# Optimization experiments

Hardware: AMD Instinct MI355X
Metric: run time of the kernel (lower is better)

Reference implementation:

```python
import jax, jax.numpy as jnp
import numpy as np
import math

B, S, L, D, H, HID = 8, 512, 6, 512, 8, 2048
N_CITIES, C = 10000, 256
IN_DIM = C + 1  # pretrained out_channels + normalized demand


def setup_inputs() -> dict:
    key = jax.random.key(0)
    ks = jax.random.split(key, 32)
    # solutions: [B,S,4]; col0 = city index (int-valued float), col2 = demand, col3 = capacity state
    idx = jax.random.randint(ks[0], (B, S), 0, N_CITIES).astype(jnp.float32)
    demand = jax.random.uniform(ks[1], (B, S), minval=0.0, maxval=10.0)
    cap_state = jax.random.uniform(ks[2], (B, S), minval=20.0, maxval=100.0)
    solutions = jnp.stack([idx, jnp.zeros((B, S)), demand, cap_state], axis=-1).astype(jnp.float32)
    capacities = jax.random.uniform(ks[3], (B,), minval=50.0, maxval=100.0)

    def lin(k, fi, fo):
        kw, kb = jax.random.split(k)
        return (jax.random.normal(kw, (fi, fo)) / np.float32(math.sqrt(fi)),
                jax.random.normal(kb, (fo,)) * 0.01)

    embeddings = jax.random.normal(ks[4], (N_CITIES, C)) * 0.1
    src_W, src_b = lin(ks[5], IN_DIM, D)
    cand_W, cand_b = lin(ks[6], IN_DIM, D)
    dep_W, dep_b = lin(ks[7], IN_DIM, D)
    feas_W, feas_b = lin(ks[8], D, 1)

    def stack(kk, fi, fo):
        Ws, bs = zip(*[lin(jax.random.fold_in(kk, i), fi, fo) for i in range(L)])
        return jnp.stack(Ws), jnp.stack(bs)

    Wq, bq = stack(ks[9], D, D)
    Wk, bk = stack(ks[10], D, D)
    Wv, bv = stack(ks[11], D, D)
    Wo, bo = stack(ks[12], D, D)
    s_scale = jnp.full((L,), 0.43, dtype=jnp.float32)
    W1, b1 = stack(ks[13], D, HID)
    W2, b2 = stack(ks[14], HID, D)
    ptr_W, ptr_b = lin(ks[15], D, 2)
    return dict(solutions=solutions, capacities=capacities, embeddings=embeddings,
                src_W=src_W, src_b=src_b, cand_W=cand_W, cand_b=cand_b,
                dep_W=dep_W, dep_b=dep_b, feas_W=feas_W, feas_b=feas_b,
                Wq=Wq, bq=bq, Wk=Wk, bk=bk, Wv=Wv, bv=bv, Wo=Wo, bo=bo,
                s_scale=s_scale, W1=W1, b1=b1, W2=W2, b2=b2,
                ptr_W=ptr_W, ptr_b=ptr_b)


def _mha(x, Wq, bq, Wk, bk, Wv, bv, Wo, bo, s):
    b, n, d = x.shape
    hd = d // H
    q = (x @ Wq + bq).reshape(b, n, H, hd)
    k = (x @ Wk + bk).reshape(b, n, H, hd)
    v = (x @ Wv + bv).reshape(b, n, H, hd)
    scores = jnp.einsum('bqhd,bkhd->bhqk', q, k) / np.float32(math.sqrt(hd))
    # ScalableSoftmax: softmax(scores + s * log(n)) over last dim
    w = jax.nn.softmax(scores + s * np.float32(math.log(n)), axis=-1)
    out = jnp.einsum('bhqk,bkhd->bqhd', w, v).reshape(b, n, d)
    return out @ Wo + bo


def _forward(solutions, capacities, embeddings, src_W, src_b, cand_W, cand_b,
             dep_W, dep_b, feas_W, feas_b, Wq, bq, Wk, bk, Wv, bv, Wo, bo,
             s_scale, W1, b1, W2, b2, ptr_W, ptr_b):
    idx = jax.lax.stop_gradient(solutions)[:, :, 0].astype(jnp.int32)  # city indices
    enc = embeddings[idx]                                              # [B,S,C]
    rem = solutions[:, 0, 3]
    nd = 2.0 * ((solutions[:, :, 2] - rem[:, None]) / capacities[:, None])
    xin = jnp.concatenate([enc, nd[..., None]], axis=-1)               # [B,S,C+1]
    xin = xin.at[:, 0, -1].set(0.0)

    # NodeEmbedder: source / candidates / depot with separate linears
    src = xin[:, :1] @ src_W + src_b
    cand = xin[:, 1:-1] @ cand_W + cand_b
    dep = xin[:, -1:] @ dep_W + dep_b
    x = jnp.concatenate([src, cand, dep], axis=1)                      # [B,S,D]

    x = x + _mha(x, Wq[0], bq[0], Wk[0], bk[0], Wv[0], bv[0], Wo[0], bo[0], s_scale[0])
    feas = (x[:, 1:-1] @ feas_W + feas_b)[..., 0]                      # [B,S-2]

    for i in range(L):
        if i > 0:
            x = x + _mha(x, Wq[i], bq[i], Wk[i], bk[i], Wv[i], bv[i], Wo[i], bo[i], s_scale[i])
        x = x + (jax.nn.relu(x @ W1[i] + b1[i]) @ W2[i] + b2[i])

    logits = x @ ptr_W + ptr_b                                         # [B,S,2]
    out = jnp.concatenate([logits[:, 1:-1, 0], logits[:, 1:-1, 1]], axis=1)  # [B,2*(S-2)]
    return out, feas


def reference(solutions, capacities, embeddings, src_W, src_b, cand_W, cand_b,
              dep_W, dep_b, feas_W, feas_b, Wq, bq, Wk, bk, Wv, bv, Wo, bo,
              s_scale, W1, b1, W2, b2, ptr_W, ptr_b):
    return _forward(solutions, capacities, embeddings, src_W, src_b, cand_W, cand_b,
                    dep_W, dep_b, feas_W, feas_b, Wq, bq, Wk, bk, Wv, bv, Wo, bo,
                    s_scale, W1, b1, W2, b2, ptr_W, ptr_b)
```

## Files before the change

### kernel.cpp

```cpp
#include <hip/hip_runtime.h>

typedef unsigned short u16;
typedef _Float16 half8 __attribute__((ext_vector_type(8)));
typedef float f32x4 __attribute__((ext_vector_type(4)));

__device__ inline float bf2f(u16 b) { return __builtin_bit_cast(float, ((unsigned)b) << 16); }
__device__ inline float h2f(u16 h) { return (float)__builtin_bit_cast(_Float16, h); }
__device__ inline u16 f2h_bits(float f) { return __builtin_bit_cast(u16, (_Float16)f); }

__device__ inline int detect_bf16(const void* caps) {
    const u16* c = (const u16*)caps;
    int cnt = 0;
#pragma unroll
    for (int k = 0; k < 4; ++k) {
        float v = bf2f(c[2 * k]);
        if (v >= 20.f && v <= 200.f) cnt++;
    }
    return cnt >= 2;
}
__device__ inline float ldin(const void* p, size_t i, int flag) {
    return flag ? bf2f(((const u16*)p)[i]) : ((const float*)p)[i];
}

#define GLOAD_LDS16(g, l)                                                              \
    __builtin_amdgcn_global_load_lds((__attribute__((address_space(1))) const void*)(g), \
                                     (__attribute__((address_space(3))) void*)(l), 16, 0, 0)

#define A_SRCW 0
#define A_SRCB 131584
#define A_CANDW 132096
#define A_CANDB 263680
#define A_DEPW 264192
#define A_DEPB 395776
#define A_FEASW 396288
#define A_FEASB 396800
#define A_PW 396801
#define A_PB 397825
#define A_BO 397827
#define A_B1 400899
#define A_B2 413187
#define A_TOTAL 416259

template <int CF, int BN>
__global__ __launch_bounds__(256) void gemm_f16(
    const u16* __restrict__ A, int lda,
    const u16* __restrict__ B, int ldb,
    void* __restrict__ Cv, int ldc,
    const float* __restrict__ bias, float* __restrict__ resid,
    u16* __restrict__ vtp,
    float scale, int relu, int N, int K)
{
    constexpr int NT = BN / 32;
    __shared__ __attribute__((aligned(16))) u16 As[2][128 * 32];
    __shared__ __attribute__((aligned(16))) u16 Bs[2][BN * 32];

    const int gx = gridDim.x, gy = gridDim.y;
    int mb, nb;
    if ((gy & 7) == 0) {
        int id = blockIdx.x + blockIdx.y * gx;
        int xcd = id & 7, local = id >> 3;
        int mloc = local / gx;
        mb = xcd * (gy >> 3) + mloc;
        nb = local - mloc * gx;
    } else {
        mb = blockIdx.y;
        nb = blockIdx.x;
    }
    const int m0 = mb * 128;
    const int n0 = nb * BN;

    const int t = threadIdx.x, lane = t & 63, wid = t >> 6;
    const int qd = lane >> 4, ml = lane & 15;
    const int wm = (wid >> 1) * 64, wn = (wid & 1) * (BN / 2);

    f32x4 acc[4][NT] = {};

    auto stage = [&](int bf, int k0) {
#pragma unroll
        for (int rep = 0; rep < 2; ++rep) {
            int seg = (wid + rep * 4) * 64 + lane;
            int row = seg >> 2, c8 = (seg & 3) * 8;
            const u16* ga = A + (long long)(m0 + row) * lda + k0 + c8;
            GLOAD_LDS16(ga, As[bf] + (size_t)(seg & ~63) * 8);
            if (BN == 128 || rep == 0) {
                int rn = n0 + row;
                if (rn > N - 1) rn = N - 1;
                const u16* gb = B + (long long)rn * ldb + k0 + c8;
                GLOAD_LDS16(gb, Bs[bf] + (size_t)(seg & ~63) * 8);
            }
        }
    };

    stage(0, 0);
    __syncthreads();

    int buf = 0;
    for (int k0 = 0; k0 < K; k0 += 32) {
        if (k0 + 32 < K) stage(buf ^ 1, k0 + 32);

        half8 af[4], bfv[NT];
#pragma unroll
        for (int mt = 0; mt < 4; ++mt)
            af[mt] = *(const half8*)(As[buf] + (wm + mt * 16 + ml) * 32 + qd * 8);
#pragma unroll
        for (int nt = 0; nt < NT; ++nt)
            bfv[nt] = *(const half8*)(Bs[buf] + (wn + nt * 16 + ml) * 32 + qd * 8);
#pragma unroll
        for (int mt = 0; mt < 4; ++mt)
#pragma unroll
            for (int nt = 0; nt < NT; ++nt)
                acc[mt][nt] = __builtin_amdgcn_mfma_f32_16x16x32_f16(af[mt], bfv[nt], acc[mt][nt], 0, 0, 0);

        __syncthreads();
        buf ^= 1;
    }

#pragma unroll
    for (int nt = 0; nt < NT; ++nt) {
        int col = n0 + wn + nt * 16 + ml;
        if (col >= N) continue;
        float bv = bias ? bias[col] : 0.f;
#pragma unroll
        for (int mt = 0; mt < 4; ++mt) {
#pragma unroll
            for (int r = 0; r < 4; ++r) {
                int rowg = m0 + wm + mt * 16 + qd * 4 + r;
                float v = acc[mt][nt][r] * scale + bv;
                if (relu) v = fmaxf(v, 0.f);
                long long off = (long long)rowg * ldc + col;
                if (CF == 1) {
                    ((float*)Cv)[off] = v;
                } else if (CF == 2) {
                    resid[off] = v;
                    ((u16*)Cv)[off] = f2h_bits(v);
                } else if (resid) {
                    float nv = resid[off] + v;
                    resid[off] = nv;
                    ((u16*)Cv)[off] = f2h_bits(nv);
                } else if (vtp && col >= 1024) {
                    int b = rowg >> 9, s = rowg & 511;
                    int cv2 = col - 1024;
                    vtp[(size_t)(((b << 3) + (cv2 >> 6)) * 32768 + (cv2 & 63) * 512 + s)] = f2h_bits(v);
                } else {
                    ((u16*)Cv)[off] = f2h_bits(v);
                }
            }
        }
    }
}

__global__ __launch_bounds__(256) void flash_k(
    const u16* __restrict__ qkv,
    const u16* __restrict__ vt,
    u16* __restrict__ ob)
{
    __shared__ __attribute__((aligned(16))) u16 Ps[128 * 136];

    int id = blockIdx.x + (blockIdx.y << 2);
    int xcd = id & 7, local = id >> 3;
    const int z = (xcd << 3) + (local >> 2);
    const int q0 = (local & 3) * 128;

    const int b = z >> 3, h = z & 7;
    const long long qbase = (long long)b * 786432;
    const u16* Q  = qkv + qbase + (long long)q0 * 1536 + h * 64;
    const u16* Kg = qkv + qbase + 512 + h * 64;
    const u16* Vg = vt + (long long)z * 32768;

    const int t = threadIdx.x, lane = t & 63, wid = t >> 6;
    const int qd = lane >> 4, ml = lane & 15;
    const int wm = wid * 32;

    half8 qf[2][2];
#pragma unroll
    for (int mt = 0; mt < 2; ++mt)
#pragma unroll
        for (int kf = 0; kf < 2; ++kf)
            qf[mt][kf] = *(const half8*)(Q + (long long)(wm + mt * 16 + ml) * 1536 + kf * 32 + qd * 8);

    f32x4 oacc[2][4] = {};
    float mrow[2][4], lrow[2][4];
#pragma unroll
    for (int mt = 0; mt < 2; ++mt)
#pragma unroll
        for (int r = 0; r < 4; ++r) { mrow[mt][r] = -3.0e38f; lrow[mt][r] = 0.f; }

    for (int kb = 0; kb < 4; ++kb) {
        f32x4 sacc[2][8] = {};
#pragma unroll
        for (int nt = 0; nt < 8; ++nt) {
#pragma unroll
            for (int kf = 0; kf < 2; ++kf) {
                half8 bf = *(const half8*)(Kg + (long long)(kb * 128 + nt * 16 + ml) * 1536 + kf * 32 + qd * 8);
#pragma unroll
                for (int mt = 0; mt < 2; ++mt)
                    sacc[mt][nt] = __builtin_amdgcn_mfma_f32_16x16x32_f16(qf[mt][kf], bf, sacc[mt][nt], 0, 0, 0);
            }
        }
#pragma unroll
        for (int mt = 0; mt < 2; ++mt) {
#pragma unroll
            for (int r = 0; r < 4; ++r) {
                float mx = -3.0e38f;
#pragma unroll
                for (int nt = 0; nt < 8; ++nt) {
                    float s = sacc[mt][nt][r] * 0.125f;
                    sacc[mt][nt][r] = s;
                    mx = fmaxf(mx, s);
                }
#pragma unroll
                for (int o = 1; o < 16; o <<= 1) mx = fmaxf(mx, __shfl_xor(mx, o, 64));
                float mnew = fmaxf(mrow[mt][r], mx);
                float alpha = __expf(mrow[mt][r] - mnew);
                mrow[mt][r] = mnew;
                lrow[mt][r] *= alpha;
#pragma unroll
                for (int nt = 0; nt < 4; ++nt) oacc[mt][nt][r] *= alpha;
                float ps = 0.f;
#pragma unroll
                for (int nt = 0; nt < 8; ++nt) {
                    float p = __expf(sacc[mt][nt][r] - mnew);
                    sacc[mt][nt][r] = p;
                    ps += p;
                }
#pragma unroll
                for (int o = 1; o < 16; o <<= 1) ps += __shfl_xor(ps, o, 64);
                lrow[mt][r] += ps;
            }
        }
#pragma unroll
        for (int mt = 0; mt < 2; ++mt)
#pragma unroll
            for (int nt = 0; nt < 8; ++nt)
#pragma unroll
                for (int r = 0; r < 4; ++r)
                    Ps[(wm + mt * 16 + qd * 4 + r) * 136 + nt * 16 + ml] = f2h_bits(sacc[mt][nt][r]);
#pragma unroll
        for (int kf = 0; kf < 4; ++kf) {
            half8 pf[2];
#pragma unroll
            for (int mt = 0; mt < 2; ++mt)
                pf[mt] = *(const half8*)(Ps + (wm + mt * 16 + ml) * 136 + kf * 32 + qd * 8);
#pragma unroll
            for (int nt = 0; nt < 4; ++nt) {
                half8 vf = *(const half8*)(Vg + (long long)(nt * 16 + ml) * 512 + kb * 128 + kf * 32 + qd * 8);
#pragma unroll
                for (int mt = 0; mt < 2; ++mt)
                    oacc[mt][nt] = __builtin_amdgcn_mfma_f32_16x16x32_f16(pf[mt], vf, oacc[mt][nt], 0, 0, 0);
            }
        }
    }

#pragma unroll
    for (int mt = 0; mt < 2; ++mt) {
#pragma unroll
        for (int r = 0; r < 4; ++r) {
            float inv = 1.f / lrow[mt][r];
            long long rowg = (long long)b * 512 + q0 + wm + mt * 16 + qd * 4 + r;
#pragma unroll
            for (int nt = 0; nt < 4; ++nt)
                ob[rowg * 512 + h * 64 + nt * 16 + ml] = f2h_bits(oacc[mt][nt][r] * inv);
        }
    }
}

template <int MODE>
__global__ void transpose_k(const void* __restrict__ src_, int s_ld, long long s_off,
                            long long s_so, long long s_si,
                            u16* __restrict__ dst, int d_ld, long long d_so, long long d_si,
                            int R, int Rs, int C, const void* caps)
{
    __shared__ u16 tile[32][33];
    const int z = blockIdx.z;
    const long long sb = s_off + (long long)(z >> 3) * s_so + (long long)(z & 7) * s_si;
    dst += (long long)(z >> 3) * d_so + (long long)(z & 7) * d_si;
    const int c0 = blockIdx.x * 32, r0 = blockIdx.y * 32;
    const int tx = threadIdx.x, ty = threadIdx.y;
    const int flag = (MODE == 1) ? detect_bf16(caps) : 0;
#pragma unroll
    for (int i = 0; i < 4; ++i) {
        int r = r0 + ty + i * 8, c = c0 + tx;
        if (r < R && c < C) {
            u16 v = 0;
            if (r < Rs) {
                size_t idx = (size_t)(sb + (long long)r * s_ld + c);
                if (MODE == 1) v = f2h_bits(ldin(src_, idx, flag));
                else           v = ((const u16*)src_)[idx];
            }
            tile[ty + i * 8][tx] = v;
        }
    }
    __syncthreads();
#pragma unroll
    for (int i = 0; i < 4; ++i) {
        int r = r0 + tx, c = c0 + ty + i * 8;
        if (r < R && c < C) dst[(long long)c * d_ld + r] = tile[tx][ty + i * 8];
    }
}

__global__ void qkvoT6_k(const void* Wq, const void* Wk, const void* Wv, const void* Wo,
                         u16* __restrict__ wqkvT6, u16* __restrict__ woT6,
                         const void* caps)
{
    __shared__ u16 tile[32][33];
    const int z = blockIdx.z;
    const int layer = z >> 2, sel = z & 3;
    const void* src = (sel == 0) ? Wq : (sel == 1) ? Wk : (sel == 2) ? Wv : Wo;
    u16* dst = (sel < 3) ? (wqkvT6 + (long long)layer * 786432 + (long long)sel * 262144)
                         : (woT6 + (long long)layer * 262144);
    const long long oW = (long long)layer * 262144;
    const int c0 = blockIdx.x * 32, r0 = blockIdx.y * 32;
    const int tx = threadIdx.x, ty = threadIdx.y;
    const int flag = detect_bf16(caps);
#pragma unroll
    for (int i = 0; i < 4; ++i) {
        int r = r0 + ty + i * 8, c = c0 + tx;
        tile[ty + i * 8][tx] = f2h_bits(ldin(src, (size_t)(oW + (long long)r * 512 + c), flag));
    }
    __syncthreads();
#pragma unroll
    for (int i = 0; i < 4; ++i) {
        int r = r0 + tx, c = c0 + ty + i * 8;
        dst[(long long)c * 512 + r] = tile[tx][ty + i * 8];
    }
}

__global__ void cvt_small_k(const void* srcW, const void* srcB, const void* candW, const void* candB,
                            const void* depW, const void* depB, const void* feasW, const void* feasB,
                            const void* pW, const void* pb, const void* boi, const void* b1i,
                            const void* b2i, const void* caps, float* __restrict__ dst)
{
    int i = blockIdx.x * 256 + threadIdx.x;
    if (i >= A_TOTAL) return;
    int flag = detect_bf16(caps);
    const void* s; int j;
    if      (i < A_SRCB)  { s = srcW;  j = i - A_SRCW; }
    else if (i < A_CANDW) { s = srcB;  j = i - A_SRCB; }
    else if (i < A_CANDB) { s = candW; j = i - A_CANDW; }
    else if (i < A_DEPW)  { s = candB; j = i - A_CANDB; }
    else if (i < A_DEPB)  { s = depW;  j = i - A_DEPW; }
    else if (i < A_FEASW) { s = depB;  j = i - A_DEPB; }
    else if (i < A_FEASB) { s = feasW; j = i - A_FEASW; }
    else if (i < A_PW)    { s = feasB; j = i - A_FEASB; }
    else if (i < A_PB)    { s = pW;    j = i - A_PW; }
    else if (i < A_BO)    { s = pb;    j = i - A_PB; }
    else if (i < A_B1)    { s = boi;   j = i - A_BO; }
    else if (i < A_B2)    { s = b1i;   j = i - A_B1; }
    else                  { s = b2i;   j = i - A_B2; }
    dst[i] = ldin(s, j, flag);
}

__global__ void catbias_k(const void* bq, const void* bk, const void* bv,
                          const void* caps, float* __restrict__ dst)
{
    int t = blockIdx.x * 256 + threadIdx.x;
    if (t >= 6 * 1536) return;
    int flag = detect_bf16(caps);
    int l = t / 1536, j = t - l * 1536;
    float v = (j < 512) ? ldin(bq, l * 512 + j, flag)
            : (j < 1024) ? ldin(bk, l * 512 + j - 512, flag)
                         : ldin(bv, l * 512 + j - 1024, flag);
    dst[t] = v;
}

__global__ __launch_bounds__(256) void gather_xin_k(
    const void* __restrict__ sol, const void* __restrict__ caps, const void* __restrict__ emb,
    u16* __restrict__ xin)
{
    const int row = blockIdx.x;
    const int b = row >> 9, s = row & 511;
    const int t = threadIdx.x;
    const int flag = detect_bf16(caps);
    float idxf = ldin(sol, (size_t)row * 4, flag);
    int idx = (int)(idxf + 0.5f);
    if (idx < 0) idx = 0;
    if (idx > 9999) idx = 9999;
    xin[(size_t)row * 288 + t] = f2h_bits(ldin(emb, (size_t)idx * 256 + t, flag));
    if (t < 32) {
        float v = 0.f;
        if (t == 0 && s != 0) {
            float rem = ldin(sol, ((size_t)b * 512) * 4 + 3, flag);
            float cap = ldin(caps, b, flag);
            float dem = ldin(sol, (size_t)row * 4 + 2, flag);
            v = 2.f * (dem - rem) / cap;
        }
        xin[(size_t)row * 288 + 256 + t] = f2h_bits(v);
    }
}

__global__ __launch_bounds__(256) void fixup_enc_k(
    const void* __restrict__ sol, const void* __restrict__ caps, const void* __restrict__ emb,
    const float* __restrict__ arena, float* __restrict__ xf, u16* __restrict__ xb)
{
    const int blk = blockIdx.x;
    const int b = blk & 7;
    const int s = (blk >> 3) ? 511 : 0;
    const int row = b * 512 + s;
    const int t = threadIdx.x;
    __shared__ float e[256];
    __shared__ float nds;
    const int flag = detect_bf16(caps);
    float idxf = ldin(sol, (size_t)row * 4, flag);
    int idx = (int)(idxf + 0.5f);
    if (idx < 0) idx = 0;
    if (idx > 9999) idx = 9999;
    e[t] = ldin(emb, (size_t)idx * 256 + t, flag);
    if (t == 0) {
        float rem = ldin(sol, ((size_t)b * 512) * 4 + 3, flag);
        float cap = ldin(caps, b, flag);
        float dem = ldin(sol, (size_t)row * 4 + 2, flag);
        nds = (s == 0) ? 0.f : 2.f * (dem - rem) / cap;
    }
    __syncthreads();
    const float* W  = (s == 0) ? arena + A_SRCW : arena + A_DEPW;
    const float* Bb = (s == 0) ? arena + A_SRCB : arena + A_DEPB;
    float a0 = 0.f, a1 = 0.f;
    for (int c = 0; c < 256; ++c) {
        float ev = e[c];
        a0 += ev * W[(size_t)c * 512 + t];
        a1 += ev * W[(size_t)c * 512 + t + 256];
    }
    float nd = nds;
    a0 += nd * W[256 * 512 + t] + Bb[t];
    a1 += nd * W[256 * 512 + t + 256] + Bb[t + 256];
    size_t o = (size_t)row * 512;
    xf[o + t] = a0;        xb[o + t] = f2h_bits(a0);
    xf[o + t + 256] = a1;  xb[o + t + 256] = f2h_bits(a1);
}

__global__ __launch_bounds__(256) void feas_k(const float* __restrict__ xf,
                                              const float* __restrict__ arena,
                                              float* __restrict__ out)
{
    int w = blockIdx.x * 4 + (threadIdx.x >> 6);
    if (w >= 8 * 510) return;
    int lane = threadIdx.x & 63;
    int b = w / 510, j = w - b * 510;
    const float* xr = xf + ((size_t)(b * 512 + 1 + j)) * 512;
    const float* fW = arena + A_FEASW;
    float a = 0.f;
#pragma unroll
    for (int i = 0; i < 8; ++i) { int d = lane + 64 * i; a += xr[d] * fW[d]; }
#pragma unroll
    for (int o = 1; o < 64; o <<= 1) a += __shfl_xor(a, o, 64);
    if (lane == 0) out[8160 + b * 510 + j] = a + arena[A_FEASB];
}

__global__ __launch_bounds__(256) void ptr_k(const float* __restrict__ xf,
                                             const float* __restrict__ arena,
                                             float* __restrict__ out)
{
    int w = blockIdx.x * 4 + (threadIdx.x >> 6);
    if (w >= 8 * 510) return;
    int lane = threadIdx.x & 63;
    int b = w / 510, j = w - b * 510;
    const float* xr = xf + ((size_t)(b * 512 + 1 + j)) * 512;
    const float* pWa = arena + A_PW;
    float a0 = 0.f, a1 = 0.f;
#pragma unroll
    for (int i = 0; i < 8; ++i) {
        int d = lane + 64 * i;
        float x = xr[d];
        a0 += x * pWa[d * 2];
        a1 += x * pWa[d * 2 + 1];
    }
#pragma unroll
    for (int o = 1; o < 64; o <<= 1) { a0 += __shfl_xor(a0, o, 64); a1 += __shfl_xor(a1, o, 64); }
    if (lane == 0) {
        out[(size_t)b * 1020 + j]       = a0 + arena[A_PB];
        out[(size_t)b * 1020 + 510 + j] = a1 + arena[A_PB + 1];
    }
}

extern "C" void kernel_launch(void* const* d_in, const int* in_sizes, int n_in,
                              void* d_out, int out_size, void* d_ws, size_t ws_size,
                              hipStream_t stream)
{
    const void* sol   = d_in[0];
    const void* caps  = d_in[1];
    const void* emb   = d_in[2];
    const void* srcW  = d_in[3];
    const void* srcB  = d_in[4];
    const void* candW = d_in[5];
    const void* candB = d_in[6];
    const void* depW  = d_in[7];
    const void* depB  = d_in[8];
    const void* feasW = d_in[9];
    const void* feasB = d_in[10];
    const void* Wq  = d_in[11];
    const void* bq  = d_in[12];
    const void* Wk  = d_in[13];
    const void* bk  = d_in[14];
    const void* Wv  = d_in[15];
    const void* bv  = d_in[16];
    const void* Wo  = d_in[17];
    const void* boi = d_in[18];
    const void* W1  = d_in[20];
    const void* b1i = d_in[21];
    const void* W2  = d_in[22];
    const void* b2i = d_in[23];
    const void* pW  = d_in[24];
    const void* pb  = d_in[25];
    float* out = (float*)d_out;

    char* w = (char*)d_ws;
    float* xf    = (float*)w; w += 8388608;
    u16* xb      = (u16*)w;   w += 4194304;
    u16* qkvb    = (u16*)w;   w += 12582912;
    u16* vt      = (u16*)w;   w += 4194304;
    u16* hb      = (u16*)w;   w += 16777216;
    u16* xin     = hb;
    u16* encW    = hb + 4096 * 288;
    u16* ob      = (u16*)w;   w += 4194304;
    u16* wqkvT6  = (u16*)w;   w += 9437184;
    u16* woT6    = (u16*)w;   w += 3145728;
    u16* w1T6    = (u16*)w;   w += 12582912;
    u16* w2T6    = (u16*)w;   w += 12582912;
    float* bqkvf = (float*)w; w += 36864;
    float* arena = (float*)w; w += A_TOTAL * 4;

    dim3 tb(32, 8);
    cvt_small_k<<<dim3((A_TOTAL + 255) / 256), 256, 0, stream>>>(
        srcW, srcB, candW, candB, depW, depB, feasW, feasB, pW, pb, boi, b1i, b2i, caps, arena);
    catbias_k<<<dim3(36), 256, 0, stream>>>(bq, bk, bv, caps, bqkvf);

    qkvoT6_k<<<dim3(16, 16, 24), tb, 0, stream>>>(Wq, Wk, Wv, Wo, wqkvT6, woT6, caps);
    transpose_k<1><<<dim3(64, 16, 6), tb, 0, stream>>>(W1, 2048, 0, 0, 1048576,
                                                       w1T6, 512, 0, 1048576, 512, 512, 2048, caps);
    transpose_k<1><<<dim3(16, 64, 6), tb, 0, stream>>>(W2, 512, 0, 0, 1048576,
                                                       w2T6, 2048, 0, 1048576, 2048, 2048, 512, caps);

    gather_xin_k<<<dim3(4096), 256, 0, stream>>>(sol, caps, emb, xin);
    transpose_k<1><<<dim3(16, 9, 1), tb, 0, stream>>>(candW, 512, 0, 0, 0,
                                                      encW, 288, 0, 0, 288, 257, 512, caps);
    gemm_f16<2, 64><<<dim3(8, 32), 256, 0, stream>>>(
        xin, 288, encW, 288,
        xb, 512, arena + A_CANDB, xf, nullptr, 1.f, 0, 512, 288);
    fixup_enc_k<<<dim3(16), 256, 0, stream>>>(sol, caps, emb, arena, xf, xb);

    for (int i = 0; i < 6; ++i) {
        gemm_f16<0, 64><<<dim3(24, 32), 256, 0, stream>>>(
            xb, 512, wqkvT6 + (long long)i * 786432, 512,
            qkvb, 1536, bqkvf + i * 1536, nullptr, vt, 1.f, 0, 1536, 512);

        flash_k<<<dim3(4, 64), 256, 0, stream>>>(qkvb, vt, ob);

        gemm_f16<0, 64><<<dim3(8, 32), 256, 0, stream>>>(
            ob, 512, woT6 + (long long)i * 262144, 512,
            xb, 512, arena + A_BO + i * 512, xf, nullptr, 1.f, 0, 512, 512);
        if (i == 0)
            feas_k<<<dim3(1020), 256, 0, stream>>>(xf, arena, out);

        gemm_f16<0, 128><<<dim3(16, 32), 256, 0, stream>>>(
            xb, 512, w1T6 + (long long)i * 1048576, 512,
            hb, 2048, arena + A_B1 + i * 2048, nullptr, nullptr, 1.f, 1, 2048, 512);

        gemm_f16<0, 64><<<dim3(8, 32), 256, 0, stream>>>(
            hb, 2048, w2T6 + (long long)i * 1048576, 2048,
            xb, 512, arena + A_B2 + i * 512, xf, nullptr, 1.f, 0, 512, 2048);
    }
    ptr_k<<<dim3(1020), 256, 0, stream>>>(xf, arena, out);
}
```

Before: 979.4 us.

## Deepen GEMM LDS pipeline to four buffers with explicit vmcnt waits

Replaces the double-buffered GEMM main loop with a four-slot LDS ring that prefetches two K-tiles ahead. Each step waits only for the oldest outstanding global-to-LDS loads (vmcnt) and uses a single raw barrier instead of a full __syncthreads per tile. This aims to hide global load latency better and cut sync overhead. In exchange it doubles LDS use, which can lower occupancy, and it depends on hand-counted vmcnt values matching the number of loads issued per stage.

```diff
diff --git a/kernel.cpp b/kernel.cpp
--- a/kernel.cpp
+++ b/kernel.cpp
@@ -25,6 +25,20 @@
 #define GLOAD_LDS16(g, l)                                                              \
     __builtin_amdgcn_global_load_lds((__attribute__((address_space(1))) const void*)(g), \
                                      (__attribute__((address_space(3))) void*)(l), 16, 0, 0)
+
+template <int N>
+__device__ inline void waitv() {
+    if constexpr (N == 0)      asm volatile("s_waitcnt vmcnt(0)" ::: "memory");
+    else if constexpr (N == 3) asm volatile("s_waitcnt vmcnt(3)" ::: "memory");
+    else if constexpr (N == 4) asm volatile("s_waitcnt vmcnt(4)" ::: "memory");
+    else if constexpr (N == 6) asm volatile("s_waitcnt vmcnt(6)" ::: "memory");
+    else if constexpr (N == 8) asm volatile("s_waitcnt vmcnt(8)" ::: "memory");
+}
+__device__ inline void barrier_raw() {
+    asm volatile("" ::: "memory");
+    __builtin_amdgcn_s_barrier();
+    asm volatile("" ::: "memory");
+}
 
 #define A_SRCW 0
 #define A_SRCB 131584
@@ -51,8 +65,9 @@
     float scale, int relu, int N, int K)
 {
     constexpr int NT = BN / 32;
-    __shared__ __attribute__((aligned(16))) u16 As[2][128 * 32];
-    __shared__ __attribute__((aligned(16))) u16 Bs[2][BN * 32];
+    constexpr int S = (BN == 128) ? 4 : 3;
+    __shared__ __attribute__((aligned(16))) u16 As[4][128 * 32];
+    __shared__ __attribute__((aligned(16))) u16 Bs[4][BN * 32];
 
     const int gx = gridDim.x, gy = gridDim.y;
     int mb, nb;
@@ -91,29 +106,42 @@
         }
     };
 
-    stage(0, 0);
-    __syncthreads();
-
-    int buf = 0;
-    for (int k0 = 0; k0 < K; k0 += 32) {
-        if (k0 + 32 < K) stage(buf ^ 1, k0 + 32);
-
+    auto compute = [&](int bf) {
         half8 af[4], bfv[NT];
 #pragma unroll
         for (int mt = 0; mt < 4; ++mt)
-            af[mt] = *(const half8*)(As[buf] + (wm + mt * 16 + ml) * 32 + qd * 8);
+            af[mt] = *(const half8*)(As[bf] + (wm + mt * 16 + ml) * 32 + qd * 8);
 #pragma unroll
         for (int nt = 0; nt < NT; ++nt)
-            bfv[nt] = *(const half8*)(Bs[buf] + (wn + nt * 16 + ml) * 32 + qd * 8);
+            bfv[nt] = *(const half8*)(Bs[bf] + (wn + nt * 16 + ml) * 32 + qd * 8);
 #pragma unroll
         for (int mt = 0; mt < 4; ++mt)
 #pragma unroll
             for (int nt = 0; nt < NT; ++nt)
                 acc[mt][nt] = __builtin_amdgcn_mfma_f32_16x16x32_f16(af[mt], bfv[nt], acc[mt][nt], 0, 0, 0);
-
-        __syncthreads();
-        buf ^= 1;
-    }
+    };
+
+    stage(0, 0);
+    if (K > 32) stage(1, 32);
+
+    int buf = 0, k0 = 0;
+    for (; k0 + 64 < K; k0 += 32) {
+        stage((buf + 2) & 3, k0 + 64);
+        waitv<2 * S>();
+        barrier_raw();
+        compute(buf);
+        buf = (buf + 1) & 3;
+    }
+    if (k0 + 32 < K) {
+        waitv<S>();
+        barrier_raw();
+        compute(buf);
+        buf = (buf + 1) & 3;
+        k0 += 32;
+    }
+    waitv<0>();
+    barrier_raw();
+    compute(buf);
 
 #pragma unroll
     for (int nt = 0; nt < NT; ++nt) {
```

New measurement: 942.9 us. 1.04x faster.

## Load GEMM fragments directly from global memory, halve M tile, add MFMA priority hints

Applied to the files above, without the earlier changes.

Removes the LDS double-buffered staging and the per-iteration barriers from the fp16 GEMM. Each wave now reads its MFMA fragments straight from global memory into registers. The M tile drops from 128 to 64 and the grids double in y to keep coverage. The flash attention kernel wraps its MFMA sections in s_setprio hints so waves favour matrix work. The GEMM trades LDS reuse between waves for more blocks and no synchronisation, so it depends on the L2 and L1 caches absorbing the duplicated global reads. The clamp on B rows past N is also dropped.

```diff
diff --git a/kernel.cpp b/kernel.cpp
--- a/kernel.cpp
+++ b/kernel.cpp
@@ -21,10 +21,6 @@
 __device__ inline float ldin(const void* p, size_t i, int flag) {
     return flag ? bf2f(((const u16*)p)[i]) : ((const float*)p)[i];
 }
-
-#define GLOAD_LDS16(g, l)                                                              \
-    __builtin_amdgcn_global_load_lds((__attribute__((address_space(1))) const void*)(g), \
-                                     (__attribute__((address_space(3))) void*)(l), 16, 0, 0)
 
 #define A_SRCW 0
 #define A_SRCB 131584
@@ -41,7 +37,7 @@
 #define A_B2 413187
 #define A_TOTAL 416259
 
-template <int CF, int BN>
+template <int CF, int BM, int BN>
 __global__ __launch_bounds__(256) void gemm_f16(
     const u16* __restrict__ A, int lda,
     const u16* __restrict__ B, int ldb,
@@ -50,9 +46,8 @@
     u16* __restrict__ vtp,
     float scale, int relu, int N, int K)
 {
-    constexpr int NT = BN / 32;
-    __shared__ __attribute__((aligned(16))) u16 As[2][128 * 32];
-    __shared__ __attribute__((aligned(16))) u16 Bs[2][BN * 32];
+    constexpr int FM = BM / 32;
+    constexpr int FN = BN / 32;
 
     const int gx = gridDim.x, gy = gridDim.y;
     int mb, nb;
@@ -66,62 +61,41 @@
         mb = blockIdx.y;
         nb = blockIdx.x;
     }
-    const int m0 = mb * 128;
+    const int m0 = mb * BM;
     const int n0 = nb * BN;
 
     const int t = threadIdx.x, lane = t & 63, wid = t >> 6;
     const int qd = lane >> 4, ml = lane & 15;
-    const int wm = (wid >> 1) * 64, wn = (wid & 1) * (BN / 2);
-
-    f32x4 acc[4][NT] = {};
-
-    auto stage = [&](int bf, int k0) {
-#pragma unroll
-        for (int rep = 0; rep < 2; ++rep) {
-            int seg = (wid + rep * 4) * 64 + lane;
-            int row = seg >> 2, c8 = (seg & 3) * 8;
-            const u16* ga = A + (long long)(m0 + row) * lda + k0 + c8;
-            GLOAD_LDS16(ga, As[bf] + (size_t)(seg & ~63) * 8);
-            if (BN == 128 || rep == 0) {
-                int rn = n0 + row;
-                if (rn > N - 1) rn = N - 1;
-                const u16* gb = B + (long long)rn * ldb + k0 + c8;
-                GLOAD_LDS16(gb, Bs[bf] + (size_t)(seg & ~63) * 8);
-            }
-        }
-    };
-
-    stage(0, 0);
-    __syncthreads();
-
-    int buf = 0;
+    const int wm = (wid >> 1) * (BM / 2), wn = (wid & 1) * (BN / 2);
+
+    const u16* Aw = A + (long long)(m0 + wm + ml) * lda + qd * 8;
+    const u16* Bw = B + (long long)(n0 + wn + ml) * ldb + qd * 8;
+
+    f32x4 acc[FM][FN] = {};
+
+#pragma unroll 2
     for (int k0 = 0; k0 < K; k0 += 32) {
-        if (k0 + 32 < K) stage(buf ^ 1, k0 + 32);
-
-        half8 af[4], bfv[NT];
-#pragma unroll
-        for (int mt = 0; mt < 4; ++mt)
-            af[mt] = *(const half8*)(As[buf] + (wm + mt * 16 + ml) * 32 + qd * 8);
-#pragma unroll
-        for (int nt = 0; nt < NT; ++nt)
-            bfv[nt] = *(const half8*)(Bs[buf] + (wn + nt * 16 + ml) * 32 + qd * 8);
-#pragma unroll
-        for (int mt = 0; mt < 4; ++mt)
-#pragma unroll
-            for (int nt = 0; nt < NT; ++nt)
+        half8 af[FM], bfv[FN];
+#pragma unroll
+        for (int mt = 0; mt < FM; ++mt)
+            af[mt] = *(const half8*)(Aw + (long long)mt * 16 * lda + k0);
+#pragma unroll
+        for (int nt = 0; nt < FN; ++nt)
+            bfv[nt] = *(const half8*)(Bw + (long long)nt * 16 * ldb + k0);
+#pragma unroll
+        for (int mt = 0; mt < FM; ++mt)
+#pragma unroll
+            for (int nt = 0; nt < FN; ++nt)
                 acc[mt][nt] = __builtin_amdgcn_mfma_f32_16x16x32_f16(af[mt], bfv[nt], acc[mt][nt], 0, 0, 0);
-
-        __syncthreads();
-        buf ^= 1;
-    }
-
-#pragma unroll
-    for (int nt = 0; nt < NT; ++nt) {
+    }
+
+#pragma unroll
+    for (int nt = 0; nt < FN; ++nt) {
         int col = n0 + wn + nt * 16 + ml;
         if (col >= N) continue;
         float bv = bias ? bias[col] : 0.f;
 #pragma unroll
-        for (int mt = 0; mt < 4; ++mt) {
+        for (int mt = 0; mt < FM; ++mt) {
 #pragma unroll
             for (int r = 0; r < 4; ++r) {
                 int rowg = m0 + wm + mt * 16 + qd * 4 + r;
@@ -187,6 +161,7 @@
 
     for (int kb = 0; kb < 4; ++kb) {
         f32x4 sacc[2][8] = {};
+        __builtin_amdgcn_s_setprio(1);
 #pragma unroll
         for (int nt = 0; nt < 8; ++nt) {
 #pragma unroll
@@ -197,6 +172,7 @@
                     sacc[mt][nt] = __builtin_amdgcn_mfma_f32_16x16x32_f16(qf[mt][kf], bf, sacc[mt][nt], 0, 0, 0);
             }
         }
+        __builtin_amdgcn_s_setprio(0);
 #pragma unroll
         for (int mt = 0; mt < 2; ++mt) {
 #pragma unroll
@@ -235,6 +211,7 @@
 #pragma unroll
                 for (int r = 0; r < 4; ++r)
                     Ps[(wm + mt * 16 + qd * 4 + r) * 136 + nt * 16 + ml] = f2h_bits(sacc[mt][nt][r]);
+        __builtin_amdgcn_s_setprio(1);
 #pragma unroll
         for (int kf = 0; kf < 4; ++kf) {
             half8 pf[2];
@@ -249,6 +226,7 @@
                     oacc[mt][nt] = __builtin_amdgcn_mfma_f32_16x16x32_f16(pf[mt], vf, oacc[mt][nt], 0, 0, 0);
             }
         }
+        __builtin_amdgcn_s_setprio(0);
     }
 
 #pragma unroll
@@ -533,29 +511,29 @@
     gather_xin_k<<<dim3(4096), 256, 0, stream>>>(sol, caps, emb, xin);
     transpose_k<1><<<dim3(16, 9, 1), tb, 0, stream>>>(candW, 512, 0, 0, 0,
                                                       encW, 288, 0, 0, 288, 257, 512, caps);
-    gemm_f16<2, 64><<<dim3(8, 32), 256, 0, stream>>>(
+    gemm_f16<2, 64, 64><<<dim3(8, 64), 256, 0, stream>>>(
         xin, 288, encW, 288,
         xb, 512, arena + A_CANDB, xf, nullptr, 1.f, 0, 512, 288);
     fixup_enc_k<<<dim3(16), 256, 0, stream>>>(sol, caps, emb, arena, xf, xb);
 
     for (int i = 0; i < 6; ++i) {
-        gemm_f16<0, 64><<<dim3(24, 32), 256, 0, stream>>>(
+        gemm_f16<0, 64, 64><<<dim3(24, 64), 256, 0, stream>>>(
             xb, 512, wqkvT6 + (long long)i * 786432, 512,
             qkvb, 1536, bqkvf + i * 1536, nullptr, vt, 1.f, 0, 1536, 512);
 
         flash_k<<<dim3(4, 64), 256, 0, stream>>>(qkvb, vt, ob);
 
-        gemm_f16<0, 64><<<dim3(8, 32), 256, 0, stream>>>(
+        gemm_f16<0, 64, 64><<<dim3(8, 64), 256, 0, stream>>>(
             ob, 512, woT6 + (long long)i * 262144, 512,
             xb, 512, arena + A_BO + i * 512, xf, nullptr, 1.f, 0, 512, 512);
         if (i == 0)
             feas_k<<<dim3(1020), 256, 0, stream>>>(xf, arena, out);
 
-        gemm_f16<0, 128><<<dim3(16, 32), 256, 0, stream>>>(
+        gemm_f16<0, 64, 128><<<dim3(16, 64), 256, 0, stream>>>(
             xb, 512, w1T6 + (long long)i * 1048576, 512,
             hb, 2048, arena + A_B1 + i * 2048, nullptr, nullptr, 1.f, 1, 2048, 512);
 
-        gemm_f16<0, 64><<<dim3(8, 32), 256, 0, stream>>>(
+        gemm_f16<0, 64, 64><<<dim3(8, 64), 256, 0, stream>>>(
             hb, 2048, w2T6 + (long long)i * 1048576, 2048,
             xb, 512, arena + A_B2 + i * 512, xf, nullptr, 1.f, 0, 512, 2048);
     }
```

Result: slower. 1.520 ms (+55.2%).
